# Kernel tuning notes

Measured on AMD Instinct MI355X. Metric: run time of the kernel, lower is better.

Reference implementation:

```python
import jax, jax.numpy as jnp
import numpy as np

N = 50000      # nodes
E = 800000     # edges
IN = 128       # in_channels
H = 128        # hidden_channels
OUT = 2        # out_channels
EA = 50        # edge_attr_channels
TC = 50        # time_channels
EPS = 1e-5     # BatchNorm eps


def setup_inputs() -> dict:
    key = jax.random.key(0)
    ks = jax.random.split(key, 24)
    d = {}
    d["x"] = jax.random.normal(ks[0], (N, IN), jnp.float32)
    d["edge_index"] = jax.random.randint(ks[1], (2, E), 0, N)
    d["edge_attr"] = jax.random.randint(ks[2], (E,), 0, 12)
    d["edge_t"] = jax.random.randint(ks[3], (E,), 0, 100000)
    d["edge_d"] = jax.random.randint(ks[4], (E,), 0, 2)

    def xavier(k, shape):
        bound = float(np.sqrt(6.0 / (shape[0] + shape[1])))
        return jax.random.uniform(k, shape, jnp.float32, -bound, bound)

    d["emb_type"] = xavier(ks[5], (12, EA))
    d["emb_dir"] = xavier(ks[6], (2, EA))
    # TimeEncoder: fixed geometric init 1/10^linspace(0,1.5,TC), zero bias
    d["w_t"] = jnp.asarray((1.0 / 10 ** np.linspace(0, 1.5, TC)).reshape(TC, 1), jnp.float32)
    d["b_t"] = jnp.zeros((TC,), jnp.float32)

    dims = [(IN, H), (H, H), (H, OUT)]  # plain mode: last layer -> out_channels
    i = 7
    for li, (din, dout) in enumerate(dims):
        fm = din + 2 * EA  # lin_m fan-in: node_dim + edge_dim*2
        bm = float(1.0 / np.sqrt(fm))
        br = float(1.0 / np.sqrt(din))
        d[f"Wm{li}"] = jax.random.uniform(ks[i], (dout, fm), jnp.float32, -bm, bm); i += 1
        d[f"bm{li}"] = jax.random.uniform(ks[i], (dout,), jnp.float32, -bm, bm); i += 1
        d[f"Wr{li}"] = jax.random.uniform(ks[i], (dout, din), jnp.float32, -br, br); i += 1
        d[f"br{li}"] = jax.random.uniform(ks[i], (dout,), jnp.float32, -br, br); i += 1
        d[f"g{li}"] = jnp.ones((dout,), jnp.float32)   # BN gamma
        d[f"be{li}"] = jnp.zeros((dout,), jnp.float32)  # BN beta
    return d


def _forward(x, emb_type, emb_dir, w_t, b_t, layers, edge_index, edge_attr, edge_t, edge_d):
    row, col = edge_index[0], edge_index[1]
    # edge embeddings: type + direction -> [E, EA]
    ea = emb_type[edge_attr] + emb_dir[edge_d]
    # time encoding: cos(Linear(log(t+1))) -> [E, TC]
    tlog = jnp.log(edge_t.astype(jnp.float32) + 1.0)
    et = jnp.cos(tlog[:, None] * w_t[:, 0][None, :] + b_t[None, :])

    h = x
    n_layers = len(layers)
    for li, (Wm, bm, Wr, br, g, be) in enumerate(layers):
        # gather + concat: [E, d + 2*EA]
        msg = jnp.concatenate([h[col], ea, et], axis=1)
        # scatter-add into node buffer (index_add_)
        agg = jax.ops.segment_sum(msg, row, num_segments=h.shape[0])
        out = 0.5 * (agg @ Wm.T + bm) + h @ Wr.T + br
        # BatchNorm1d (training-mode batch stats, biased variance)
        mu = out.mean(axis=0)
        var = out.var(axis=0)
        out = (out - mu) * jax.lax.rsqrt(var + EPS) * g + be
        if li != n_layers - 1:
            out = jax.nn.elu(out)  # dropout = identity in eval
        h = out
    return jax.nn.log_softmax(h, axis=-1)


def reference(x, edge_index, edge_attr, edge_t, edge_d,
              emb_type, emb_dir, w_t, b_t,
              Wm0, bm0, Wr0, br0, g0, be0,
              Wm1, bm1, Wr1, br1, g1, be1,
              Wm2, bm2, Wr2, br2, g2, be2):
    layers = [(Wm0, bm0, Wr0, br0, g0, be0),
              (Wm1, bm1, Wr1, br1, g1, be1),
              (Wm2, bm2, Wr2, br2, g2, be2)]
    return _forward(x, emb_type, emb_dir, w_t, b_t, layers,
                    edge_index, edge_attr, edge_t, edge_d)
```

## Files before the change

### kernel.cpp

```cpp
#include <hip/hip_runtime.h>
#include <math.h>

#define N_NODES 50000
#define N_EDGES 800000
#define DIN 128
#define DH 128
#define EA_C 50
#define DE 100
#define FM 228
#define AS 320
#define WKL 384
#define BM 32
#define BN_EPS 1e-5f
#define SCAN_NB ((N_NODES + 255) / 256)
#define GBLK ((N_NODES + BM - 1) / BM)
#define GSZ  ((N_NODES + 7) / 8)

typedef __attribute__((ext_vector_type(8))) short short8;
typedef __attribute__((ext_vector_type(4))) short s16x4;
typedef __attribute__((ext_vector_type(4))) float f32x4;
typedef unsigned int u32;
typedef unsigned short u16;

__device__ inline u16 f2bf(float f) {
  u32 u = __float_as_uint(f);
  u32 r = (u + 0x7fffu + ((u >> 16) & 1u)) >> 16;
  return (u16)r;
}
__device__ inline float bf2f(u16 h) { return __uint_as_float(((u32)h) << 16); }
__device__ inline u32 pack_hl(float v) {
  u16 hi = f2bf(v);
  u16 lo = f2bf(v - bf2f(hi));
  return (u32)hi | ((u32)lo << 16);
}
__device__ inline float unpack_hl(u32 p) {
  return bf2f((u16)(p & 0xffffu)) + bf2f((u16)(p >> 16));
}

__global__ void k_count(const int* __restrict__ row, const int* __restrict__ col,
                        const int* __restrict__ attr, const int* __restrict__ dire,
                        const int* __restrict__ tim,
                        int* __restrict__ counts, uint2* __restrict__ pay8) {
  int e = blockIdx.x * 256 + threadIdx.x;
  if (e < N_EDGES) {
    atomicAdd(&counts[row[e]], 1);
    uint2 rec;
    rec.x = (u32)col[e] | ((u32)attr[e] << 16) | ((u32)dire[e] << 20);
    rec.y = __float_as_uint(__logf((float)tim[e] + 1.0f));
    pay8[e] = rec;
  }
}

__global__ void k_scan_a(const int* __restrict__ counts, int* __restrict__ incl,
                         int* __restrict__ bsum) {
  __shared__ int buf[256];
  int i = blockIdx.x * 256 + threadIdx.x;
  int v = (i < N_NODES) ? counts[i] : 0;
  buf[threadIdx.x] = v;
  __syncthreads();
#pragma unroll
  for (int off = 1; off < 256; off <<= 1) {
    int t = (threadIdx.x >= off) ? buf[threadIdx.x - off] : 0;
    __syncthreads();
    buf[threadIdx.x] += t;
    __syncthreads();
  }
  if (i < N_NODES) incl[i] = buf[threadIdx.x];
  if (threadIdx.x == 255) bsum[blockIdx.x] = buf[255];
}

__global__ void k_scan_b(const int* __restrict__ bsum, int* __restrict__ boff,
                         int* __restrict__ row_ptr) {
  __shared__ int buf[256];
  int v = (threadIdx.x < SCAN_NB) ? bsum[threadIdx.x] : 0;
  buf[threadIdx.x] = v;
  __syncthreads();
#pragma unroll
  for (int off = 1; off < 256; off <<= 1) {
    int t = (threadIdx.x >= off) ? buf[threadIdx.x - off] : 0;
    __syncthreads();
    buf[threadIdx.x] += t;
    __syncthreads();
  }
  if (threadIdx.x < SCAN_NB) boff[threadIdx.x] = buf[threadIdx.x] - v;
  if (threadIdx.x == 255) row_ptr[N_NODES] = buf[255];
}

__global__ void k_scan_c(const int* __restrict__ incl, const int* __restrict__ counts,
                         const int* __restrict__ boff, int* __restrict__ row_ptr,
                         int* __restrict__ cursor) {
  int i = blockIdx.x * 256 + threadIdx.x;
  if (i < N_NODES) {
    int p = incl[i] - counts[i] + boff[blockIdx.x];
    row_ptr[i] = p;
    cursor[i] = p;
  }
}

__global__ void k_fill(const int* __restrict__ row, const uint2* __restrict__ pay8,
                       int* __restrict__ cursor, uint2* __restrict__ er_s) {
  int b = blockIdx.x;
  int g = b & 7, c = b >> 3;
  int e = c * 256 + threadIdx.x;
  if (e >= N_EDGES) return;
  int r = row[e];
  int lo = g * GSZ;
  if (r < lo || r >= lo + GSZ) return;
  int slot = atomicAdd(&cursor[r], 1);
  er_s[slot] = pay8[e];
}

__global__ void k_conv_x(const float* __restrict__ x, u32* __restrict__ A) {
  int idx = blockIdx.x * 256 + threadIdx.x;
  if (idx >= N_NODES * DH) return;
  int n = idx >> 7, c = idx & 127;
  ((u16*)(A + (size_t)n * AS + 128))[c] = f2bf(x[idx]);
}

__global__ void k_aggHE(const int* __restrict__ row_ptr, const uint2* __restrict__ er_s,
                        const float* __restrict__ emb_type, const float* __restrict__ emb_dir,
                        const float* __restrict__ w_t, const float* __restrict__ b_t,
                        u32* __restrict__ A) {
  int wave = threadIdx.x >> 6, lane = threadIdx.x & 63;
  int n = blockIdx.x * 4 + wave;
  if (n >= N_NODES) return;
  int s = row_ptr[n], epos = row_ptr[n + 1];
  bool ew = lane < EA_C;
  float wt = ew ? w_t[lane] : 0.f;
  float bt = ew ? b_t[lane] : 0.f;
  float ax = 0.f, ay = 0.f, ea = 0.f, et = 0.f;
  int p = s;
  for (; p + 1 < epos; p += 2) {
    uint2 r0 = er_s[p], r1 = er_s[p + 1];
    u32 v0 = A[(size_t)(r0.x & 0xffff) * AS + 128 + lane];
    u32 v1 = A[(size_t)(r1.x & 0xffff) * AS + 128 + lane];
    if (ew) {
      ea += emb_type[((r0.x >> 16) & 0xF) * EA_C + lane] + emb_dir[(r0.x >> 20) * EA_C + lane];
      ea += emb_type[((r1.x >> 16) & 0xF) * EA_C + lane] + emb_dir[(r1.x >> 20) * EA_C + lane];
      et += __cosf(__uint_as_float(r0.y) * wt + bt);
      et += __cosf(__uint_as_float(r1.y) * wt + bt);
    }
    ax += bf2f((u16)(v0 & 0xffffu)) + bf2f((u16)(v1 & 0xffffu));
    ay += bf2f((u16)(v0 >> 16)) + bf2f((u16)(v1 >> 16));
  }
  if (p < epos) {
    uint2 r0 = er_s[p];
    u32 v0 = A[(size_t)(r0.x & 0xffff) * AS + 128 + lane];
    if (ew) {
      ea += emb_type[((r0.x >> 16) & 0xF) * EA_C + lane] + emb_dir[(r0.x >> 20) * EA_C + lane];
      et += __cosf(__uint_as_float(r0.y) * wt + bt);
    }
    ax += bf2f((u16)(v0 & 0xffffu));
    ay += bf2f((u16)(v0 >> 16));
  }
  uint2 o; o.x = pack_hl(ax); o.y = pack_hl(ay);
  *reinterpret_cast<uint2*>(A + (size_t)n * AS + 2 * lane) = o;
  if (ew) {
    A[(size_t)n * AS + 192 + lane] = pack_hl(ea);
    A[(size_t)n * AS + 242 + lane] = pack_hl(et);
  } else {
    int l = lane - EA_C;
    A[(size_t)n * AS + 292 + l] = 0u;
    A[(size_t)n * AS + 306 + l] = 0u;
  }
}

__global__ void k_aggH(const int* __restrict__ row_ptr, const uint2* __restrict__ er_s,
                       u32* __restrict__ A) {
  int wave = threadIdx.x >> 6, lane = threadIdx.x & 63;
  int n = blockIdx.x * 4 + wave;
  if (n >= N_NODES) return;
  int s = row_ptr[n], epos = row_ptr[n + 1];
  float ax = 0.f, ay = 0.f;
  int p = s;
  for (; p + 3 < epos; p += 4) {
    int c0 = er_s[p].x & 0xffff, c1 = er_s[p + 1].x & 0xffff;
    int c2 = er_s[p + 2].x & 0xffff, c3 = er_s[p + 3].x & 0xffff;
    u32 v0 = A[(size_t)c0 * AS + 128 + lane];
    u32 v1 = A[(size_t)c1 * AS + 128 + lane];
    u32 v2 = A[(size_t)c2 * AS + 128 + lane];
    u32 v3 = A[(size_t)c3 * AS + 128 + lane];
    ax += bf2f((u16)(v0 & 0xffffu)) + bf2f((u16)(v1 & 0xffffu)) +
          bf2f((u16)(v2 & 0xffffu)) + bf2f((u16)(v3 & 0xffffu));
    ay += bf2f((u16)(v0 >> 16)) + bf2f((u16)(v1 >> 16)) +
          bf2f((u16)(v2 >> 16)) + bf2f((u16)(v3 >> 16));
  }
  for (; p < epos; ++p) {
    u32 v = A[(size_t)(er_s[p].x & 0xffff) * AS + 128 + lane];
    ax += bf2f((u16)(v & 0xffffu));
    ay += bf2f((u16)(v >> 16));
  }
  uint2 o; o.x = pack_hl(ax); o.y = pack_hl(ay);
  *reinterpret_cast<uint2*>(A + (size_t)n * AS + 2 * lane) = o;
}

__global__ void k_wprep(const float* __restrict__ Wm, const float* __restrict__ Wr,
                        u32* __restrict__ WT2) {
  int idx = blockIdx.x * 256 + threadIdx.x;
  if (idx >= DH * WKL) return;
  int o = idx / WKL, k = idx - o * WKL;
  float v;
  if (k < 128) v = 0.5f * Wm[o * FM + k];
  else if (k < 256) v = Wr[o * DIN + (k - 128)];
  else if (k < 356) v = 0.5f * Wm[o * FM + (k - 128)];
  else v = 0.f;
  WT2[idx] = pack_hl(v);
}

__global__ void k_bias(const float* __restrict__ bm, const float* __restrict__ br,
                       float* __restrict__ bv) {
  int o = threadIdx.x;
  if (o < DH) bv[o] = 0.5f * bm[o] + br[o];
}

__global__ __launch_bounds__(256) void k_mfma(const u32* __restrict__ A,
                                              const u32* __restrict__ W,
                                              const float* __restrict__ bv,
                                              float* __restrict__ out,
                                              float* __restrict__ pstat) {
  __shared__ u16 Ah[BM][32], Al[BM][32];
  __shared__ u16 Wh[128][32], Wl[128][32];
  __shared__ float sred[4][128], qred[4][128];
  int tid = threadIdx.x;
  int wv = tid >> 6, ln = tid & 63;
  int rw = wv >> 1, cw = wv & 1;
  int colb = ln & 15, fq = ln >> 4;
  int node0 = blockIdx.x * BM;

  {
    float* sp = &sred[0][0]; float* qp = &qred[0][0];
    sp[tid] = 0.f; sp[tid + 256] = 0.f;
    qp[tid] = 0.f; qp[tid + 256] = 0.f;
  }

  f32x4 acc[4];
#pragma unroll
  for (int nt = 0; nt < 4; ++nt) acc[nt] = (f32x4){0.f, 0.f, 0.f, 0.f};

  int ar = tid >> 3, aq = tid & 7;
  int an = node0 + ar;
  bool valid = an < N_NODES;
  const u32* aptr = A + (size_t)an * AS;
  int wc = tid >> 1, wk = (tid & 1) * 16;
  const u32* wptr = W + (size_t)wc * WKL + wk;

  const u16* afh = &Ah[(rw << 4) + colb][fq * 8];
  const u16* afl = &Al[(rw << 4) + colb][fq * 8];

#pragma unroll
  for (int ch = 0; ch < 12; ++ch) {
    const int kl = ch * 32;
    const bool ph2 = (ch >= 4 && ch < 8);
    uint4 a0 = make_uint4(0, 0, 0, 0);
    if (!ph2) {
      int acol = (ch < 4 ? kl : kl - 64) + aq * 4;
      if (valid) a0 = *reinterpret_cast<const uint4*>(aptr + acol);
    } else if (aq < 4) {
      int acol = 128 + ((kl - 128) >> 1) + aq * 4;
      if (valid) a0 = *reinterpret_cast<const uint4*>(aptr + acol);
    }
    uint4 w0 = *reinterpret_cast<const uint4*>(wptr + kl);
    uint4 w1 = *reinterpret_cast<const uint4*>(wptr + kl + 4);
    uint4 w2 = *reinterpret_cast<const uint4*>(wptr + kl + 8);
    uint4 w3 = *reinterpret_cast<const uint4*>(wptr + kl + 12);

    __syncthreads();

    if (!ph2) {
      u32 va[4] = {a0.x, a0.y, a0.z, a0.w};
      s16x4 h, l;
#pragma unroll
      for (int j = 0; j < 4; ++j) { h[j] = (short)(va[j] & 0xffffu); l[j] = (short)(va[j] >> 16); }
      *reinterpret_cast<s16x4*>(&Ah[ar][aq * 4]) = h;
      *reinterpret_cast<s16x4*>(&Al[ar][aq * 4]) = l;
    } else if (aq < 4) {
      *reinterpret_cast<short8*>(&Ah[ar][aq * 8]) = *reinterpret_cast<const short8*>(&a0);
    }
    {
      u32 vw[16] = {w0.x, w0.y, w0.z, w0.w, w1.x, w1.y, w1.z, w1.w,
                    w2.x, w2.y, w2.z, w2.w, w3.x, w3.y, w3.z, w3.w};
      short8 h0, l0, h1, l1;
#pragma unroll
      for (int j = 0; j < 8; ++j) {
        h0[j] = (short)(vw[j] & 0xffffu);     l0[j] = (short)(vw[j] >> 16);
        h1[j] = (short)(vw[j + 8] & 0xffffu); l1[j] = (short)(vw[j + 8] >> 16);
      }
      *reinterpret_cast<short8*>(&Wh[wc][wk]) = h0;
      *reinterpret_cast<short8*>(&Wh[wc][wk + 8]) = h1;
      *reinterpret_cast<short8*>(&Wl[wc][wk]) = l0;
      *reinterpret_cast<short8*>(&Wl[wc][wk + 8]) = l1;
    }

    __syncthreads();

    short8 ah = *reinterpret_cast<const short8*>(afh);
    short8 al = *reinterpret_cast<const short8*>(afl);
#pragma unroll
    for (int nt = 0; nt < 4; ++nt) {
      int wrow = (cw << 6) + nt * 16 + colb;
      short8 bh = *reinterpret_cast<const short8*>(&Wh[wrow][fq * 8]);
      short8 bl = *reinterpret_cast<const short8*>(&Wl[wrow][fq * 8]);
      acc[nt] = __builtin_amdgcn_mfma_f32_16x16x32_bf16(ah, bh, acc[nt], 0, 0, 0);
      if (!ph2) acc[nt] = __builtin_amdgcn_mfma_f32_16x16x32_bf16(al, bh, acc[nt], 0, 0, 0);
      acc[nt] = __builtin_amdgcn_mfma_f32_16x16x32_bf16(ah, bl, acc[nt], 0, 0, 0);
    }
  }

  int rbase = node0 + (rw << 4) + (fq << 2);
#pragma unroll
  for (int nt = 0; nt < 4; ++nt) {
    int col = (cw << 6) + nt * 16 + colb;
    float bb = bv[col];
    float s = 0.f, q = 0.f;
#pragma unroll
    for (int r = 0; r < 4; ++r) {
      int n = rbase + r;
      if (n < N_NODES) {
        float v = acc[nt][r] + bb;
        out[(size_t)n * DH + col] = v;
        s += v; q += v * v;
      }
    }
    s += __shfl_xor(s, 16, 64); s += __shfl_xor(s, 32, 64);
    q += __shfl_xor(q, 16, 64); q += __shfl_xor(q, 32, 64);
    if (fq == 0) { sred[wv][col] = s; qred[wv][col] = q; }
  }
  __syncthreads();
  if (tid < 128) {
    float s = sred[0][tid] + sred[1][tid] + sred[2][tid] + sred[3][tid];
    float q = qred[0][tid] + qred[1][tid] + qred[2][tid] + qred[3][tid];
    pstat[(size_t)blockIdx.x * 256 + tid] = s;
    pstat[(size_t)blockIdx.x * 256 + 128 + tid] = q;
  }
}

__global__ void k_bnred(const float* __restrict__ pstat, float* __restrict__ stats) {
  __shared__ float red[256];
  int slot = blockIdx.x;
  float s = 0.f;
  for (int b = threadIdx.x; b < GBLK; b += 256) s += pstat[(size_t)b * 256 + slot];
  red[threadIdx.x] = s;
  __syncthreads();
  for (int off = 128; off >= 1; off >>= 1) {
    if (threadIdx.x < off) red[threadIdx.x] += red[threadIdx.x + off];
    __syncthreads();
  }
  if (threadIdx.x == 0) stats[slot] = red[0];
}

__global__ void k_bnapply(const float* __restrict__ x, const float* __restrict__ stats,
                          const float* __restrict__ g, const float* __restrict__ be,
                          u32* __restrict__ A) {
  int idx = blockIdx.x * 256 + threadIdx.x;
  if (idx >= N_NODES * DH) return;
  int n = idx >> 7, c = idx & 127;
  float mu = stats[c] * (1.0f / N_NODES);
  float var = stats[128 + c] * (1.0f / N_NODES) - mu * mu;
  float y = (x[idx] - mu) * rsqrtf(var + BN_EPS) * g[c] + be[c];
  y = y > 0.f ? y : expm1f(y);
  ((u16*)(A + (size_t)n * AS + 128))[c] = f2bf(y);
}

__global__ void k_l2_dense(const u32* __restrict__ A,
                           const float* __restrict__ Wm2, const float* __restrict__ bm2,
                           const float* __restrict__ Wr2, const float* __restrict__ br2,
                           float* __restrict__ val, float* __restrict__ pm) {
  int wave = threadIdx.x >> 6, lane = threadIdx.x & 63;
  int n = blockIdx.x * 4 + wave;
  if (n >= N_NODES) return;
  const u32* ar = A + (size_t)n * AS;
  const u16* h16 = (const u16*)(ar + 128);
  float h0 = bf2f(h16[lane]);
  float h1 = bf2f(h16[lane + 64]);
  float e0 = unpack_hl(ar[192 + lane]);
  float e1 = (lane < DE - 64) ? unpack_hl(ar[256 + lane]) : 0.f;

  float pm0 = h0 * Wm2[lane] + h1 * Wm2[lane + 64];
  float pm1 = h0 * Wm2[FM + lane] + h1 * Wm2[FM + lane + 64];
  float ve0 = e0 * Wm2[DIN + lane] + ((lane < DE - 64) ? e1 * Wm2[DIN + lane + 64] : 0.f);
  float ve1 = e0 * Wm2[FM + DIN + lane] + ((lane < DE - 64) ? e1 * Wm2[FM + DIN + lane + 64] : 0.f);
  float pr0 = h0 * Wr2[lane] + h1 * Wr2[lane + 64];
  float pr1 = h0 * Wr2[DH + lane] + h1 * Wr2[DH + lane + 64];

#pragma unroll
  for (int m = 32; m >= 1; m >>= 1) {
    pm0 += __shfl_xor(pm0, m, 64); pm1 += __shfl_xor(pm1, m, 64);
    ve0 += __shfl_xor(ve0, m, 64); ve1 += __shfl_xor(ve1, m, 64);
    pr0 += __shfl_xor(pr0, m, 64); pr1 += __shfl_xor(pr1, m, 64);
  }
  if (lane == 0) {
    val[n * 2 + 0] = 0.5f * (ve0 + bm2[0]) + pr0 + br2[0];
    val[n * 2 + 1] = 0.5f * (ve1 + bm2[1]) + pr1 + br2[1];
    pm[n * 2 + 0] = pm0;
    pm[n * 2 + 1] = pm1;
  }
}

__global__ void k_agg2(const int* __restrict__ row_ptr, const uint2* __restrict__ er_s,
                       const float* __restrict__ pm, float* __restrict__ val) {
  int n = blockIdx.x * 256 + threadIdx.x;
  if (n >= N_NODES) return;
  float a0 = 0.f, a1 = 0.f;
  int s = row_ptr[n], e = row_ptr[n + 1];
  for (int p = s; p < e; ++p) {
    int c = er_s[p].x & 0xffff;
    a0 += pm[c * 2]; a1 += pm[c * 2 + 1];
  }
  val[n * 2] += 0.5f * a0;
  val[n * 2 + 1] += 0.5f * a1;
}

__global__ void k_bnstats2(const float* __restrict__ val, float* __restrict__ s4) {
  float s0 = 0.f, q0 = 0.f, s1 = 0.f, q1 = 0.f;
  for (int n = blockIdx.x * 256 + threadIdx.x; n < N_NODES; n += gridDim.x * 256) {
    float v0 = val[n * 2], v1 = val[n * 2 + 1];
    s0 += v0; q0 += v0 * v0; s1 += v1; q1 += v1 * v1;
  }
  __shared__ float b[256][4];
  b[threadIdx.x][0] = s0; b[threadIdx.x][1] = q0;
  b[threadIdx.x][2] = s1; b[threadIdx.x][3] = q1;
  __syncthreads();
  for (int off = 128; off >= 1; off >>= 1) {
    if (threadIdx.x < off)
      for (int j = 0; j < 4; ++j) b[threadIdx.x][j] += b[threadIdx.x + off][j];
    __syncthreads();
  }
  if (threadIdx.x == 0)
    for (int j = 0; j < 4; ++j) atomicAdd(&s4[j], b[0][j]);
}

__global__ void k_final(const float* __restrict__ val, const float* __restrict__ s4,
                        const float* __restrict__ g2, const float* __restrict__ be2,
                        float* __restrict__ out) {
  int n = blockIdx.x * 256 + threadIdx.x;
  if (n >= N_NODES) return;
  float mu0 = s4[0] * (1.f / N_NODES), var0 = s4[1] * (1.f / N_NODES) - mu0 * mu0;
  float mu1 = s4[2] * (1.f / N_NODES), var1 = s4[3] * (1.f / N_NODES) - mu1 * mu1;
  float y0 = (val[n * 2] - mu0) * rsqrtf(var0 + BN_EPS) * g2[0] + be2[0];
  float y1 = (val[n * 2 + 1] - mu1) * rsqrtf(var1 + BN_EPS) * g2[1] + be2[1];
  float m = fmaxf(y0, y1);
  float lse = m + __logf(__expf(y0 - m) + __expf(y1 - m));
  out[n * 2] = y0 - lse;
  out[n * 2 + 1] = y1 - lse;
}

extern "C" void kernel_launch(void* const* d_in, const int* in_sizes, int n_in,
                              void* d_out, int out_size, void* d_ws, size_t ws_size,
                              hipStream_t stream) {
  (void)in_sizes; (void)n_in; (void)out_size; (void)ws_size;
  const float* x        = (const float*)d_in[0];
  const int*   eidx     = (const int*)d_in[1];
  const int*   row      = eidx;
  const int*   col      = eidx + N_EDGES;
  const int*   attr     = (const int*)d_in[2];
  const int*   tim      = (const int*)d_in[3];
  const int*   dire     = (const int*)d_in[4];
  const float* emb_type = (const float*)d_in[5];
  const float* emb_dir  = (const float*)d_in[6];
  const float* w_t      = (const float*)d_in[7];
  const float* b_t      = (const float*)d_in[8];
  const float* Wm[3] = {(const float*)d_in[9],  (const float*)d_in[15], (const float*)d_in[21]};
  const float* bm[3] = {(const float*)d_in[10], (const float*)d_in[16], (const float*)d_in[22]};
  const float* Wr[3] = {(const float*)d_in[11], (const float*)d_in[17], (const float*)d_in[23]};
  const float* br[3] = {(const float*)d_in[12], (const float*)d_in[18], (const float*)d_in[24]};
  const float* g[3]  = {(const float*)d_in[13], (const float*)d_in[19], (const float*)d_in[25]};
  const float* be[3] = {(const float*)d_in[14], (const float*)d_in[20], (const float*)d_in[26]};
  float* out = (float*)d_out;

  char* p = (char*)d_ws;
  u32* A     = (u32*)p;   p += sizeof(u32) * (size_t)N_NODES * AS;
  float* gout = (float*)p; p += sizeof(float) * (size_t)N_NODES * DH;
  uint2* er_s = (uint2*)p; p += sizeof(uint2) * (size_t)N_EDGES;
  float* pstat = (float*)p; p += sizeof(float) * (size_t)GBLK * 256;
  u32* WT2[2];
  WT2[0] = (u32*)p; p += sizeof(u32) * DH * WKL;
  WT2[1] = (u32*)p; p += sizeof(u32) * DH * WKL;
  float* bv[2];
  bv[0] = (float*)p; p += sizeof(float) * DH;
  bv[1] = (float*)p; p += sizeof(float) * DH;
  float* val  = (float*)p;  p += sizeof(float) * (size_t)N_NODES * 2;
  float* pmb  = (float*)p;  p += sizeof(float) * (size_t)N_NODES * 2;
  float* stats = (float*)p; p += sizeof(float) * 520;
  int* counts  = (int*)p;   p += sizeof(int) * N_NODES;
  int* cursor  = (int*)p;   p += sizeof(int) * N_NODES;
  int* row_ptr = (int*)p;   p += sizeof(int) * (N_NODES + 1);
  int* incl    = (int*)p;   p += sizeof(int) * N_NODES;
  int* bsum    = (int*)p;   p += sizeof(int) * SCAN_NB;
  int* boff    = (int*)p;   p += sizeof(int) * SCAN_NB;

  uint2* pay8 = (uint2*)gout;

  const int EB = (N_EDGES + 255) / 256;
  const int NB = (N_NODES + 255) / 256;
  const int AB = (N_NODES + 3) / 4;
  const int XB = (N_NODES * DH + 255) / 256;
  const int WB = (DH * WKL + 255) / 256;

  hipMemsetAsync(counts, 0, sizeof(int) * N_NODES, stream);
  hipMemsetAsync(stats, 0, sizeof(float) * 520, stream);

  k_count<<<EB, 256, 0, stream>>>(row, col, attr, dire, tim, counts, pay8);
  k_scan_a<<<SCAN_NB, 256, 0, stream>>>(counts, incl, bsum);
  k_scan_b<<<1, 256, 0, stream>>>(bsum, boff, row_ptr);
  k_scan_c<<<SCAN_NB, 256, 0, stream>>>(incl, counts, boff, row_ptr, cursor);
  k_fill<<<8 * EB, 256, 0, stream>>>(row, pay8, cursor, er_s);

  for (int l = 0; l < 2; ++l) {
    k_wprep<<<WB, 256, 0, stream>>>(Wm[l], Wr[l], WT2[l]);
    k_bias<<<1, 128, 0, stream>>>(bm[l], br[l], bv[l]);
  }

  k_conv_x<<<XB, 256, 0, stream>>>(x, A);

  k_aggHE<<<AB, 256, 0, stream>>>(row_ptr, er_s, emb_type, emb_dir, w_t, b_t, A);
  k_mfma<<<GBLK, 256, 0, stream>>>(A, WT2[0], bv[0], gout, pstat);
  k_bnred<<<256, 256, 0, stream>>>(pstat, stats);
  k_bnapply<<<XB, 256, 0, stream>>>(gout, stats, g[0], be[0], A);

  k_aggH<<<AB, 256, 0, stream>>>(row_ptr, er_s, A);
  k_mfma<<<GBLK, 256, 0, stream>>>(A, WT2[1], bv[1], gout, pstat);
  k_bnred<<<256, 256, 0, stream>>>(pstat, stats + 256);
  k_bnapply<<<XB, 256, 0, stream>>>(gout, stats + 256, g[1], be[1], A);

  k_l2_dense<<<AB, 256, 0, stream>>>(A, Wm[2], bm[2], Wr[2], br[2], val, pmb);
  k_agg2<<<NB, 256, 0, stream>>>(row_ptr, er_s, pmb, val);
  k_bnstats2<<<64, 256, 0, stream>>>(val, stats + 512);
  k_final<<<NB, 256, 0, stream>>>(val, stats + 512, g[2], be[2], out);
}
```

Baseline: 358.9 us.

## Precompute gather offsets, deepen gather unroll, vectorize conversion and BN-apply kernels

Edge records now store the source node index pre-multiplied by the row stride, so gather kernels skip the multiply, and the attr/dir fields move to the upper bits. The aggregation loops are unrolled further (4 in aggHE, 8 in aggH) so more independent gathers are in flight at once. k_conv_x and k_bnapply process four channels per thread using float4 loads and 8-byte stores. k_agg2 recovers the node index with a multiply-high divide by 320, which adds a few ALU ops there and requires col*320 to fit in 24 bits.

```diff
diff --git a/kernel.cpp b/kernel.cpp
--- a/kernel.cpp
+++ b/kernel.cpp
@@ -45,7 +45,7 @@
   if (e < N_EDGES) {
     atomicAdd(&counts[row[e]], 1);
     uint2 rec;
-    rec.x = (u32)col[e] | ((u32)attr[e] << 16) | ((u32)dire[e] << 20);
+    rec.x = (u32)col[e] * AS | ((u32)attr[e] << 24) | ((u32)dire[e] << 28);
     rec.y = __float_as_uint(__logf((float)tim[e] + 1.0f));
     pay8[e] = rec;
   }
@@ -112,9 +112,13 @@
 
 __global__ void k_conv_x(const float* __restrict__ x, u32* __restrict__ A) {
   int idx = blockIdx.x * 256 + threadIdx.x;
-  if (idx >= N_NODES * DH) return;
-  int n = idx >> 7, c = idx & 127;
-  ((u16*)(A + (size_t)n * AS + 128))[c] = f2bf(x[idx]);
+  if (idx >= N_NODES * 32) return;
+  int n = idx >> 5, c4 = (idx & 31) << 2;
+  float4 v = *reinterpret_cast<const float4*>(x + (size_t)n * DH + c4);
+  uint2 o;
+  o.x = (u32)f2bf(v.x) | ((u32)f2bf(v.y) << 16);
+  o.y = (u32)f2bf(v.z) | ((u32)f2bf(v.w) << 16);
+  *reinterpret_cast<uint2*>(A + (size_t)n * AS + 128 + (c4 >> 1)) = o;
 }
 
 __global__ void k_aggHE(const int* __restrict__ row_ptr, const uint2* __restrict__ er_s,
@@ -130,24 +134,30 @@
   float bt = ew ? b_t[lane] : 0.f;
   float ax = 0.f, ay = 0.f, ea = 0.f, et = 0.f;
   int p = s;
-  for (; p + 1 < epos; p += 2) {
-    uint2 r0 = er_s[p], r1 = er_s[p + 1];
-    u32 v0 = A[(size_t)(r0.x & 0xffff) * AS + 128 + lane];
-    u32 v1 = A[(size_t)(r1.x & 0xffff) * AS + 128 + lane];
+  for (; p + 3 < epos; p += 4) {
+    uint2 r0 = er_s[p], r1 = er_s[p + 1], r2 = er_s[p + 2], r3 = er_s[p + 3];
+    u32 v0 = A[(r0.x & 0xFFFFFFu) + 128 + lane];
+    u32 v1 = A[(r1.x & 0xFFFFFFu) + 128 + lane];
+    u32 v2 = A[(r2.x & 0xFFFFFFu) + 128 + lane];
+    u32 v3 = A[(r3.x & 0xFFFFFFu) + 128 + lane];
     if (ew) {
-      ea += emb_type[((r0.x >> 16) & 0xF) * EA_C + lane] + emb_dir[(r0.x >> 20) * EA_C + lane];
-      ea += emb_type[((r1.x >> 16) & 0xF) * EA_C + lane] + emb_dir[(r1.x >> 20) * EA_C + lane];
-      et += __cosf(__uint_as_float(r0.y) * wt + bt);
-      et += __cosf(__uint_as_float(r1.y) * wt + bt);
-    }
-    ax += bf2f((u16)(v0 & 0xffffu)) + bf2f((u16)(v1 & 0xffffu));
-    ay += bf2f((u16)(v0 >> 16)) + bf2f((u16)(v1 >> 16));
-  }
-  if (p < epos) {
+      ea += emb_type[((r0.x >> 24) & 0xF) * EA_C + lane] + emb_dir[(r0.x >> 28) * EA_C + lane];
+      ea += emb_type[((r1.x >> 24) & 0xF) * EA_C + lane] + emb_dir[(r1.x >> 28) * EA_C + lane];
+      ea += emb_type[((r2.x >> 24) & 0xF) * EA_C + lane] + emb_dir[(r2.x >> 28) * EA_C + lane];
+      ea += emb_type[((r3.x >> 24) & 0xF) * EA_C + lane] + emb_dir[(r3.x >> 28) * EA_C + lane];
+      et += __cosf(__uint_as_float(r0.y) * wt + bt) + __cosf(__uint_as_float(r1.y) * wt + bt);
+      et += __cosf(__uint_as_float(r2.y) * wt + bt) + __cosf(__uint_as_float(r3.y) * wt + bt);
+    }
+    ax += bf2f((u16)(v0 & 0xffffu)) + bf2f((u16)(v1 & 0xffffu)) +
+          bf2f((u16)(v2 & 0xffffu)) + bf2f((u16)(v3 & 0xffffu));
+    ay += bf2f((u16)(v0 >> 16)) + bf2f((u16)(v1 >> 16)) +
+          bf2f((u16)(v2 >> 16)) + bf2f((u16)(v3 >> 16));
+  }
+  for (; p < epos; ++p) {
     uint2 r0 = er_s[p];
-    u32 v0 = A[(size_t)(r0.x & 0xffff) * AS + 128 + lane];
+    u32 v0 = A[(r0.x & 0xFFFFFFu) + 128 + lane];
     if (ew) {
-      ea += emb_type[((r0.x >> 16) & 0xF) * EA_C + lane] + emb_dir[(r0.x >> 20) * EA_C + lane];
+      ea += emb_type[((r0.x >> 24) & 0xF) * EA_C + lane] + emb_dir[(r0.x >> 28) * EA_C + lane];
       et += __cosf(__uint_as_float(r0.y) * wt + bt);
     }
     ax += bf2f((u16)(v0 & 0xffffu));
@@ -173,20 +183,18 @@
   int s = row_ptr[n], epos = row_ptr[n + 1];
   float ax = 0.f, ay = 0.f;
   int p = s;
-  for (; p + 3 < epos; p += 4) {
-    int c0 = er_s[p].x & 0xffff, c1 = er_s[p + 1].x & 0xffff;
-    int c2 = er_s[p + 2].x & 0xffff, c3 = er_s[p + 3].x & 0xffff;
-    u32 v0 = A[(size_t)c0 * AS + 128 + lane];
-    u32 v1 = A[(size_t)c1 * AS + 128 + lane];
-    u32 v2 = A[(size_t)c2 * AS + 128 + lane];
-    u32 v3 = A[(size_t)c3 * AS + 128 + lane];
-    ax += bf2f((u16)(v0 & 0xffffu)) + bf2f((u16)(v1 & 0xffffu)) +
-          bf2f((u16)(v2 & 0xffffu)) + bf2f((u16)(v3 & 0xffffu));
-    ay += bf2f((u16)(v0 >> 16)) + bf2f((u16)(v1 >> 16)) +
-          bf2f((u16)(v2 >> 16)) + bf2f((u16)(v3 >> 16));
+  for (; p + 7 < epos; p += 8) {
+    u32 v[8];
+#pragma unroll
+    for (int j = 0; j < 8; ++j) v[j] = A[(er_s[p + j].x & 0xFFFFFFu) + 128 + lane];
+#pragma unroll
+    for (int j = 0; j < 8; ++j) {
+      ax += bf2f((u16)(v[j] & 0xffffu));
+      ay += bf2f((u16)(v[j] >> 16));
+    }
   }
   for (; p < epos; ++p) {
-    u32 v = A[(size_t)(er_s[p].x & 0xffff) * AS + 128 + lane];
+    u32 v = A[(er_s[p].x & 0xFFFFFFu) + 128 + lane];
     ax += bf2f((u16)(v & 0xffffu));
     ay += bf2f((u16)(v >> 16));
   }
@@ -352,13 +360,31 @@
                           const float* __restrict__ g, const float* __restrict__ be,
                           u32* __restrict__ A) {
   int idx = blockIdx.x * 256 + threadIdx.x;
-  if (idx >= N_NODES * DH) return;
-  int n = idx >> 7, c = idx & 127;
-  float mu = stats[c] * (1.0f / N_NODES);
-  float var = stats[128 + c] * (1.0f / N_NODES) - mu * mu;
-  float y = (x[idx] - mu) * rsqrtf(var + BN_EPS) * g[c] + be[c];
-  y = y > 0.f ? y : expm1f(y);
-  ((u16*)(A + (size_t)n * AS + 128))[c] = f2bf(y);
+  if (idx >= N_NODES * 32) return;
+  int n = idx >> 5, c4 = (idx & 31) << 2;
+  float4 v = *reinterpret_cast<const float4*>(x + (size_t)n * DH + c4);
+  float4 sm = *reinterpret_cast<const float4*>(stats + c4);
+  float4 sq = *reinterpret_cast<const float4*>(stats + 128 + c4);
+  float4 gg = *reinterpret_cast<const float4*>(g + c4);
+  float4 bb = *reinterpret_cast<const float4*>(be + c4);
+  float vv[4] = {v.x, v.y, v.z, v.w};
+  float mm[4] = {sm.x, sm.y, sm.z, sm.w};
+  float qq[4] = {sq.x, sq.y, sq.z, sq.w};
+  float ga[4] = {gg.x, gg.y, gg.z, gg.w};
+  float ba[4] = {bb.x, bb.y, bb.z, bb.w};
+  u16 ob[4];
+#pragma unroll
+  for (int j = 0; j < 4; ++j) {
+    float mu = mm[j] * (1.0f / N_NODES);
+    float var = qq[j] * (1.0f / N_NODES) - mu * mu;
+    float y = (vv[j] - mu) * rsqrtf(var + BN_EPS) * ga[j] + ba[j];
+    y = y > 0.f ? y : expm1f(y);
+    ob[j] = f2bf(y);
+  }
+  uint2 o;
+  o.x = (u32)ob[0] | ((u32)ob[1] << 16);
+  o.y = (u32)ob[2] | ((u32)ob[3] << 16);
+  *reinterpret_cast<uint2*>(A + (size_t)n * AS + 128 + (c4 >> 1)) = o;
 }
 
 __global__ void k_l2_dense(const u32* __restrict__ A,
@@ -403,7 +429,8 @@
   float a0 = 0.f, a1 = 0.f;
   int s = row_ptr[n], e = row_ptr[n + 1];
   for (int p = s; p < e; ++p) {
-    int c = er_s[p].x & 0xffff;
+    u32 coff = er_s[p].x & 0xFFFFFFu;
+    u32 c = __umulhi(coff >> 6, 0xCCCCCCCDu) >> 2;
     a0 += pm[c * 2]; a1 += pm[c * 2 + 1];
   }
   val[n * 2] += 0.5f * a0;
@@ -493,7 +520,7 @@
   const int EB = (N_EDGES + 255) / 256;
   const int NB = (N_NODES + 255) / 256;
   const int AB = (N_NODES + 3) / 4;
-  const int XB = (N_NODES * DH + 255) / 256;
+  const int XB4 = (N_NODES * 32 + 255) / 256;
   const int WB = (DH * WKL + 255) / 256;
 
   hipMemsetAsync(counts, 0, sizeof(int) * N_NODES, stream);
@@ -510,17 +537,17 @@
     k_bias<<<1, 128, 0, stream>>>(bm[l], br[l], bv[l]);
   }
 
-  k_conv_x<<<XB, 256, 0, stream>>>(x, A);
+  k_conv_x<<<XB4, 256, 0, stream>>>(x, A);
 
   k_aggHE<<<AB, 256, 0, stream>>>(row_ptr, er_s, emb_type, emb_dir, w_t, b_t, A);
   k_mfma<<<GBLK, 256, 0, stream>>>(A, WT2[0], bv[0], gout, pstat);
   k_bnred<<<256, 256, 0, stream>>>(pstat, stats);
-  k_bnapply<<<XB, 256, 0, stream>>>(gout, stats, g[0], be[0], A);
+  k_bnapply<<<XB4, 256, 0, stream>>>(gout, stats, g[0], be[0], A);
 
   k_aggH<<<AB, 256, 0, stream>>>(row_ptr, er_s, A);
   k_mfma<<<GBLK, 256, 0, stream>>>(A, WT2[1], bv[1], gout, pstat);
   k_bnred<<<256, 256, 0, stream>>>(pstat, stats + 256);
-  k_bnapply<<<XB, 256, 0, stream>>>(gout, stats + 256, g[1], be[1], A);
+  k_bnapply<<<XB4, 256, 0, stream>>>(gout, stats + 256, g[1], be[1], A);
 
   k_l2_dense<<<AB, 256, 0, stream>>>(A, Wm[2], bm[2], Wr[2], br[2], val, pmb);
   k_agg2<<<NB, 256, 0, stream>>>(row_ptr, er_s, pmb, val);
```

Measured after the change: 334.5 us. -6.8%, faster.
